# Kernel optimization log

Measured on AMD Instinct MI355X. Metric: run time of the kernel, lower is better.

Reference implementation:

```python
import jax, jax.numpy as jnp
import numpy as np

EPS = 1e-5  # BatchNorm eps; eval mode with default running stats (mean=0, var=1)


def _bn(h, gamma, beta):
    # eval-mode BatchNorm2d with running_mean=0, running_var=1
    scale = gamma / jnp.sqrt(1.0 + EPS)
    return h * scale[None, :, None, None] + beta[None, :, None, None]


def _conv1x1(h, w, b):
    # 1x1 conv == channel matmul. h: [B,C,H,W], w: [O,C], b: [O]
    return jnp.einsum('bchw,oc->bohw', h, w) + b[None, :, None, None]


def setup_inputs() -> dict:
    key = jax.random.key(0)
    ks = jax.random.split(key, 16)
    B, C, H, W = 8, 64, 64, 64
    inp = {
        'x': jax.random.normal(ks[0], (B, C, H, W), dtype=jnp.float32),
        'saliency_map': jax.random.uniform(ks[1], (B, H, W), dtype=jnp.float32),
    }
    i = 2
    for name in ('q', 'k', 'v'):
        inp[f'w_{name}'] = jax.random.normal(ks[i], (C, C), dtype=jnp.float32) * (1.0 / np.sqrt(C)); i += 1
        inp[f'b_{name}'] = jax.random.normal(ks[i], (C,), dtype=jnp.float32) * 0.02; i += 1
        inp[f'g_{name}'] = 1.0 + 0.1 * jax.random.normal(ks[i], (C,), dtype=jnp.float32); i += 1
        inp[f'be_{name}'] = jax.random.normal(ks[i], (C,), dtype=jnp.float32) * 0.02; i += 1
    inp['g_o'] = 1.0 + 0.1 * jax.random.normal(ks[14], (C,), dtype=jnp.float32)
    inp['be_o'] = jax.random.normal(ks[15], (C,), dtype=jnp.float32) * 0.02
    return inp


def reference(x, saliency_map, w_q, b_q, g_q, be_q, w_k, b_k, g_k, be_k,
              w_v, b_v, g_v, be_v, g_o, be_o):
    B, C, H, W = x.shape
    HW = H * W
    query = _bn(_conv1x1(x, w_q, b_q), g_q, be_q).reshape(B, C, HW)
    key_ = _bn(_conv1x1(x, w_k, b_k), g_k, be_k).reshape(B, C, HW)
    value = _bn(_conv1x1(x, w_v, b_v), g_v, be_v).reshape(B, C, HW)
    mask = saliency_map.reshape(B, 1, HW)  # broadcast over channels == repeat
    query = query * mask
    # scores[b,i,j] = sum_c q[b,c,i] * k[b,c,j]; softmax over j (no scaling)
    scores = jnp.einsum('bci,bcj->bij', query, key_)
    attn = jax.nn.softmax(scores, axis=-1)
    # out[b,c,j] = sum_i v[b,c,i] * attn[b,i,j]
    enhanced = jnp.einsum('bci,bij->bcj', value, attn).reshape(B, C, H, W)
    enhanced = enhanced + x
    return _bn(enhanced, g_o, be_o)
```

## Files before the change

### kernel.cpp

```cpp
#include <hip/hip_runtime.h>

#define EPS 1e-5f
#define LOG2E 1.4426950408889634f

typedef __attribute__((ext_vector_type(8)))  short    s8b;
typedef __attribute__((ext_vector_type(4)))  short    s4b;
typedef __attribute__((ext_vector_type(16))) float    f32x16;
typedef __attribute__((ext_vector_type(4)))  float    f32x4;
typedef __attribute__((ext_vector_type(4)))  unsigned u32x4;

__device__ __forceinline__ unsigned cvt_pk_bf16(float lo, float hi) {
    unsigned r;
    asm("v_cvt_pk_bf16_f32 %0, %1, %2" : "=v"(r) : "v"(lo), "v"(hi));
    return r;
}
__device__ __forceinline__ void permswap(unsigned &a, unsigned &b) {
    asm("v_permlane32_swap_b32 %0, %1" : "+v"(a), "+v"(b));
}
union PackAB { u32x4 u; s8b s; };

__device__ __forceinline__ unsigned short f2bf(float f) {
    union { float f; unsigned u; } v; v.f = f;
    unsigned r = v.u + 0x7FFFu + ((v.u >> 16) & 1u);
    return (unsigned short)(r >> 16);
}
__device__ __forceinline__ float bf2f(unsigned short h) {
    union { unsigned u; float f; } v; v.u = ((unsigned)h) << 16;
    return v.f;
}


__global__ __launch_bounds__(256) void qkv_kernel(
    const float* __restrict__ x, const float* __restrict__ sal,
    const float* __restrict__ wq, const float* __restrict__ bq,
    const float* __restrict__ gq, const float* __restrict__ beq,
    const float* __restrict__ wk, const float* __restrict__ bk,
    const float* __restrict__ gk, const float* __restrict__ bek,
    const float* __restrict__ wv, const float* __restrict__ bv,
    const float* __restrict__ gv, const float* __restrict__ bev,
    short* __restrict__ Qf, short* __restrict__ Kf, short* __restrict__ Vf)
{
    __shared__ short wbf[6][4096];
    __shared__ short xbf[4096];
    __shared__ short v_lds[4096];
    __shared__ float sc_lds[3][64];
    __shared__ float bb_lds[3][64];

    const int t = threadIdx.x;
    const int b = blockIdx.x & 7;
    const int p0 = (blockIdx.x >> 3) * 64;

    if (t < 192) {
        int m = t >> 6, o = t & 63;
        const float* g  = (m == 0) ? gq  : (m == 1) ? gk  : gv;
        const float* be = (m == 0) ? beq : (m == 1) ? bek : bev;
        const float* bi = (m == 0) ? bq  : (m == 1) ? bk  : bv;
        float lam = (m == 0) ? LOG2E : 1.0f;
        float s = g[o] * rsqrtf(1.0f + EPS) * lam;
        sc_lds[m][o] = s;
        bb_lds[m][o] = bi[o] * s + be[o] * lam;
    }
    __syncthreads();

    for (int rep = 0; rep < 12; ++rep) {
        int idx = (rep * 256 + t) * 4;
        int m = idx >> 12;
        int r = idx & 4095;
        int o = r >> 6, c0 = r & 63;
        const float* w = (m == 0) ? wq : (m == 1) ? wk : wv;
        float4 v4 = *reinterpret_cast<const float4*>(w + r);
        float s = sc_lds[m][o];
        float w0 = v4.x * s, w1 = v4.y * s, w2 = v4.z * s, w3 = v4.w * s;
        unsigned short h0 = f2bf(w0), h1 = f2bf(w1), h2 = f2bf(w2), h3 = f2bf(w3);
        s4b hv, lv;
        hv[0] = (short)h0; hv[1] = (short)h1; hv[2] = (short)h2; hv[3] = (short)h3;
        lv[0] = (short)f2bf(w0 - bf2f(h0));
        lv[1] = (short)f2bf(w1 - bf2f(h1));
        lv[2] = (short)f2bf(w2 - bf2f(h2));
        lv[3] = (short)f2bf(w3 - bf2f(h3));
        int sidx = (o * 64 + c0) ^ ((o & 7) << 3);
        *reinterpret_cast<s4b*>(&wbf[m * 2 + 0][sidx]) = hv;
        *reinterpret_cast<s4b*>(&wbf[m * 2 + 1][sidx]) = lv;
    }
    {
        const int xp = t & 63;
        const int cgrp = (t >> 6) * 4;
        const float* xb = x + ((size_t)(b * 64) << 12) + p0 + xp;
        for (int rep = 0; rep < 4; ++rep) {
            int cb = cgrp + rep * 16;
            float x0 = xb[(size_t)(cb + 0) << 12];
            float x1 = xb[(size_t)(cb + 1) << 12];
            float x2 = xb[(size_t)(cb + 2) << 12];
            float x3 = xb[(size_t)(cb + 3) << 12];
            s4b pk;
            pk[0] = (short)f2bf(x0); pk[1] = (short)f2bf(x1);
            pk[2] = (short)f2bf(x2); pk[3] = (short)f2bf(x3);
            int sidx = (xp * 64 + cb) ^ ((xp & 7) << 3);
            *reinterpret_cast<s4b*>(&xbf[sidx]) = pk;
        }
    }
    __syncthreads();

    const int lane = t & 63, wave = t >> 6;
    const int l31 = lane & 31, hi = lane >> 5;
    const int phalf = wave & 1, ohalf = wave >> 1;
    const int prow = phalf * 32 + l31;
    const int orow = ohalf * 32 + l31;
    const int ib = (p0 >> 5) + phalf;
    const int swz = (l31 & 7) << 3;

    s8b bx[4];
#pragma unroll
    for (int s = 0; s < 4; ++s)
        bx[s] = *reinterpret_cast<const s8b*>(
            &xbf[(prow * 64 + s * 16 + hi * 8) ^ ((prow & 7) << 3)]);

    const float msk = sal[(((size_t)b) << 12) + p0 + prow];

#pragma unroll
    for (int m = 0; m < 3; ++m) {
        s8b ah[4], al[4];
#pragma unroll
        for (int s = 0; s < 4; ++s) {
            int sidx = (orow * 64 + s * 16 + hi * 8) ^ swz;
            ah[s] = *reinterpret_cast<const s8b*>(&wbf[m * 2 + 0][sidx]);
            al[s] = *reinterpret_cast<const s8b*>(&wbf[m * 2 + 1][sidx]);
        }
        f32x16 d;
#pragma unroll
        for (int r = 0; r < 16; ++r) d[r] = 0.f;
#pragma unroll
        for (int s = 0; s < 4; ++s)
            d = __builtin_amdgcn_mfma_f32_32x32x16_bf16(ah[s], bx[s], d, 0, 0, 0);
#pragma unroll
        for (int s = 0; s < 4; ++s)
            d = __builtin_amdgcn_mfma_f32_32x32x16_bf16(al[s], bx[s], d, 0, 0, 0);

        float pv[16];
#pragma unroll
        for (int g = 0; g < 4; ++g) {
            f32x4 bb = *reinterpret_cast<const f32x4*>(
                &bb_lds[m][ohalf * 32 + 8 * g + 4 * hi]);
#pragma unroll
            for (int q = 0; q < 4; ++q) pv[g * 4 + q] = d[g * 4 + q] + bb[q];
        }
        if (m == 0) {
#pragma unroll
            for (int r = 0; r < 16; ++r) pv[r] *= msk;
        }
        if (m < 2) {
            unsigned a0 = cvt_pk_bf16(pv[0],  pv[1]);
            unsigned a1 = cvt_pk_bf16(pv[2],  pv[3]);
            unsigned a2 = cvt_pk_bf16(pv[4],  pv[5]);
            unsigned a3 = cvt_pk_bf16(pv[6],  pv[7]);
            unsigned b0 = cvt_pk_bf16(pv[8],  pv[9]);
            unsigned b1 = cvt_pk_bf16(pv[10], pv[11]);
            unsigned b2 = cvt_pk_bf16(pv[12], pv[13]);
            unsigned b3 = cvt_pk_bf16(pv[14], pv[15]);
            permswap(a0, a2); permswap(a1, a3);
            permswap(b0, b2); permswap(b1, b3);
            PackAB pa0, pa1;
            pa0.u.x = a0; pa0.u.y = a1; pa0.u.z = a2; pa0.u.w = a3;
            pa1.u.x = b0; pa1.u.y = b1; pa1.u.z = b2; pa1.u.w = b3;
            short* dst = (m == 0) ? Qf : Kf;
            size_t base =
                ((((size_t)(b * 128 + ib) * 4 + ohalf * 2) * 2 + hi) * 32 + l31) * 8;
            *reinterpret_cast<u32x4*>(dst + base)       = pa0.u;
            *reinterpret_cast<u32x4*>(dst + base + 512) = pa1.u;
        } else {
#pragma unroll
            for (int r = 0; r < 16; ++r) {
                int c = ohalf * 32 + (r & 3) + 8 * (r >> 2) + 4 * hi;
                int sidx = (c * 64 + prow) ^ ((c & 7) << 3);
                v_lds[sidx] = (short)f2bf(pv[r]);
            }
        }
    }
    __syncthreads();

    const size_t vbase = (size_t)(b * 128 + (p0 >> 5)) * 2048;
#pragma unroll
    for (int r = 0; r < 2; ++r) {
        int f = r * 256 + t;
        int c = f & 63;
        int iL = ((f >> 6) & 7) * 8;
        int sidx = (c * 64 + iL) ^ ((c & 7) << 3);
        u32x4 val = *reinterpret_cast<const u32x4*>(&v_lds[sidx]);
        *reinterpret_cast<u32x4*>(Vf + vbase + (size_t)f * 8) = val;
    }
}

#define LOADK(JB, DST) {                                                      \
    const short* _kp = Kf +                                                   \
        ((((size_t)(b * 128 + (JB)) * 4) * 2 + hi) * 32 + l31) * 8;           \
    DST[0] = *reinterpret_cast<const s8b*>(_kp);                              \
    DST[1] = *reinterpret_cast<const s8b*>(_kp + 512);                        \
    DST[2] = *reinterpret_cast<const s8b*>(_kp + 1024);                       \
    DST[3] = *reinterpret_cast<const s8b*>(_kp + 1536); }

#define RBODY(KARR) {                                                         \
    f32x16 sacc;                                                              \
    _Pragma("unroll") for (int r = 0; r < 16; ++r) sacc[r] = 0.f;             \
    __builtin_amdgcn_s_setprio(1);                                            \
    _Pragma("unroll") for (int s = 0; s < 4; ++s)                             \
        sacc = __builtin_amdgcn_mfma_f32_32x32x16_bf16(qf[s], KARR[s], sacc, 0, 0, 0); \
    __builtin_amdgcn_s_setprio(0);                                            \
    _Pragma("unroll") for (int r = 0; r < 16; ++r)                            \
        lsum[r] += __builtin_exp2f(sacc[r]); }

__global__ __launch_bounds__(512, 2) void rowsum_kernel(
    const short* __restrict__ Qf, const short* __restrict__ Kf,
    float* __restrict__ inv_l)
{
    __shared__ float part[8][32];

    const int t = threadIdx.x;
    const int b = blockIdx.x & 7;
    const int it2 = blockIdx.x >> 3;
    const int wave = t >> 6, lane = t & 63;
    const int wi = wave & 1, wj = wave >> 1;
    const int l31 = lane & 31, hi = lane >> 5;

    const short* qp = Qf +
        ((((size_t)(b * 128 + it2 * 2 + wi) * 4) * 2 + hi) * 32 + l31) * 8;
    s8b qf[4];
#pragma unroll
    for (int s = 0; s < 4; ++s)
        qf[s] = *reinterpret_cast<const s8b*>(qp + s * 512);

    float lsum[16];
#pragma unroll
    for (int r = 0; r < 16; ++r) lsum[r] = 0.f;

    s8b kA[4], kB[4];
    LOADK(wj, kA);
    for (int jj = 0; jj < 32; jj += 2) {
        LOADK((jj + 1) * 4 + wj, kB);
        RBODY(kA);
        if (jj + 2 < 32) { LOADK((jj + 2) * 4 + wj, kA); }
        RBODY(kB);
    }

#pragma unroll
    for (int off = 1; off < 32; off <<= 1)
#pragma unroll
        for (int r = 0; r < 16; ++r) lsum[r] += __shfl_xor(lsum[r], off);

    if (l31 == 0) {
#pragma unroll
        for (int r = 0; r < 16; ++r) {
            int iloc = (r & 3) + 8 * (r >> 2) + 4 * hi;
            part[wave][iloc] = lsum[r];
        }
    }
    __syncthreads();
    if (t < 64) {
        int wi_t = t >> 5, row = t & 31;
        float s = part[wi_t][row] + part[2 + wi_t][row] +
                  part[4 + wi_t][row] + part[6 + wi_t][row];
        inv_l[(((size_t)b) << 12) + it2 * 64 + wi_t * 32 + row] = 1.0f / s;
    }
}

#define LOADQ(IB, DST) {                                                      \
    const short* _qp = Qf +                                                   \
        ((((size_t)(b * 128 + (IB)) * 4) * 2 + hi) * 32 + l31) * 8;           \
    DST[0] = *reinterpret_cast<const s8b*>(_qp);                              \
    DST[1] = *reinterpret_cast<const s8b*>(_qp + 512);                        \
    DST[2] = *reinterpret_cast<const s8b*>(_qp + 1024);                       \
    DST[3] = *reinterpret_cast<const s8b*>(_qp + 1536); }

#define LOADV(IB, DST) {                                                      \
    const short* _vp = Vf +                                                   \
        ((((size_t)(b * 128 + (IB)) * 2) * 2 + hi) * 64 + l31) * 8;           \
    DST[0] = *reinterpret_cast<const s8b*>(_vp);                              \
    DST[1] = *reinterpret_cast<const s8b*>(_vp + 256);                        \
    DST[2] = *reinterpret_cast<const s8b*>(_vp + 1024);                       \
    DST[3] = *reinterpret_cast<const s8b*>(_vp + 1280); }

#define ABODY(QARR, VARR, IB) {                                               \
    f32x16 sacc;                                                              \
    _Pragma("unroll") for (int r = 0; r < 16; ++r) sacc[r] = 0.f;             \
    __builtin_amdgcn_s_setprio(1);                                            \
    _Pragma("unroll") for (int s = 0; s < 4; ++s)                             \
        sacc = __builtin_amdgcn_mfma_f32_32x32x16_bf16(QARR[s], kf[s], sacc, 0, 0, 0); \
    __builtin_amdgcn_s_setprio(0);                                            \
    float p[16];                                                              \
    const int _ibase = (IB) * 32 + 4 * hi;                                    \
    _Pragma("unroll") for (int g = 0; g < 4; ++g) {                           \
        f32x4 li = *reinterpret_cast<const f32x4*>(lip + _ibase + 8 * g);     \
        _Pragma("unroll") for (int q = 0; q < 4; ++q)                         \
            p[g * 4 + q] = __builtin_exp2f(sacc[g * 4 + q]) * li[q];          \
    }                                                                         \
    unsigned a0 = cvt_pk_bf16(p[0],  p[1]),  a1 = cvt_pk_bf16(p[2],  p[3]);   \
    unsigned a2 = cvt_pk_bf16(p[4],  p[5]),  a3 = cvt_pk_bf16(p[6],  p[7]);   \
    unsigned b0 = cvt_pk_bf16(p[8],  p[9]),  b1 = cvt_pk_bf16(p[10], p[11]);  \
    unsigned b2 = cvt_pk_bf16(p[12], p[13]), b3 = cvt_pk_bf16(p[14], p[15]);  \
    permswap(a0, a2); permswap(a1, a3); permswap(b0, b2); permswap(b1, b3);   \
    PackAB pa0, pa1;                                                          \
    pa0.u.x = a0; pa0.u.y = a1; pa0.u.z = a2; pa0.u.w = a3;                   \
    pa1.u.x = b0; pa1.u.y = b1; pa1.u.z = b2; pa1.u.w = b3;                   \
    __builtin_amdgcn_s_setprio(1);                                            \
    acc0 = __builtin_amdgcn_mfma_f32_32x32x16_bf16(pa0.s, VARR[0], acc0, 0, 0, 0); \
    acc1 = __builtin_amdgcn_mfma_f32_32x32x16_bf16(pa0.s, VARR[1], acc1, 0, 0, 0); \
    acc0 = __builtin_amdgcn_mfma_f32_32x32x16_bf16(pa1.s, VARR[2], acc0, 0, 0, 0); \
    acc1 = __builtin_amdgcn_mfma_f32_32x32x16_bf16(pa1.s, VARR[3], acc1, 0, 0, 0); \
    __builtin_amdgcn_s_setprio(0); }

__global__ __launch_bounds__(512, 2) void attnout_kernel(
    const short* __restrict__ Qf, const short* __restrict__ Kf,
    const short* __restrict__ Vf, const float* __restrict__ inv_l,
    const float* __restrict__ x, const float* __restrict__ go,
    const float* __restrict__ beo, float* __restrict__ out)
{
    __shared__ float red[2][3][64][33];

    const int t = threadIdx.x;
    const int b = blockIdx.x & 7;
    const int jt = blockIdx.x >> 3;
    const int wave = t >> 6, lane = t & 63;
    const int wr = wave >> 1;
    const int wc = wave & 1;
    const int l31 = lane & 31, hi = lane >> 5;

    const short* kp = Kf +
        ((((size_t)(b * 128 + jt * 2 + wc) * 4) * 2 + hi) * 32 + l31) * 8;
    s8b kf[4];
#pragma unroll
    for (int s = 0; s < 4; ++s)
        kf[s] = *reinterpret_cast<const s8b*>(kp + s * 512);

    f32x16 acc0, acc1;
#pragma unroll
    for (int r = 0; r < 16; ++r) { acc0[r] = 0.f; acc1[r] = 0.f; }

    const float* lip = inv_l + (((size_t)b) << 12);

    s8b qA[4], qB[4], vA[4], vB[4];
    LOADQ(wr, qA);
    LOADV(wr, vA);
    for (int ii = 0; ii < 32; ii += 2) {
        const int ibA = ii * 4 + wr;
        const int ibB = ibA + 4;
        LOADQ(ibB, qB);
        LOADV(ibB, vB);
        ABODY(qA, vA, ibA);
        if (ii + 2 < 32) { LOADQ(ibA + 8, qA); LOADV(ibA + 8, vA); }
        ABODY(qB, vB, ibB);
    }

    if (wr > 0) {
#pragma unroll
        for (int nf = 0; nf < 2; ++nf) {
            const f32x16& A = nf ? acc1 : acc0;
            int c = nf * 32 + l31;
#pragma unroll
            for (int g = 0; g < 4; ++g) {
                f32x4 v;
                v.x = A[g * 4 + 0]; v.y = A[g * 4 + 1];
                v.z = A[g * 4 + 2]; v.w = A[g * 4 + 3];
                *reinterpret_cast<f32x4*>(&red[wc][wr - 1][c][g * 8 + 4 * hi]) = v;
            }
        }
    }
    __syncthreads();
    if (wr == 0) {
#pragma unroll
        for (int nf = 0; nf < 2; ++nf) {
            const f32x16& A = nf ? acc1 : acc0;
            int c = nf * 32 + l31;
            const float sc = go[c] * rsqrtf(1.0f + EPS);
            const float bb = beo[c];
            size_t rowb = (((size_t)(b * 64 + c)) << 12) + jt * 64 + wc * 32;
#pragma unroll
            for (int g = 0; g < 4; ++g) {
                int jl = g * 8 + 4 * hi;
                f32x4 p0 = *reinterpret_cast<const f32x4*>(&red[wc][0][c][jl]);
                f32x4 p1 = *reinterpret_cast<const f32x4*>(&red[wc][1][c][jl]);
                f32x4 p2 = *reinterpret_cast<const f32x4*>(&red[wc][2][c][jl]);
                f32x4 xv = *reinterpret_cast<const f32x4*>(x + rowb + jl);
                f32x4 ov;
                ov.x = (A[g * 4 + 0] + p0.x + p1.x + p2.x + xv.x) * sc + bb;
                ov.y = (A[g * 4 + 1] + p0.y + p1.y + p2.y + xv.y) * sc + bb;
                ov.z = (A[g * 4 + 2] + p0.z + p1.z + p2.z + xv.z) * sc + bb;
                ov.w = (A[g * 4 + 3] + p0.w + p1.w + p2.w + xv.w) * sc + bb;
                *reinterpret_cast<f32x4*>(out + rowb + jl) = ov;
            }
        }
    }
}

extern "C" void kernel_launch(void* const* d_in, const int* in_sizes, int n_in,
                              void* d_out, int out_size, void* d_ws, size_t ws_size,
                              hipStream_t stream)
{
    (void)in_sizes; (void)n_in; (void)out_size; (void)ws_size;
    const float* x   = (const float*)d_in[0];
    const float* sal = (const float*)d_in[1];
    const float* wq  = (const float*)d_in[2];  const float* bq  = (const float*)d_in[3];
    const float* gq  = (const float*)d_in[4];  const float* beq = (const float*)d_in[5];
    const float* wk  = (const float*)d_in[6];  const float* bk  = (const float*)d_in[7];
    const float* gk  = (const float*)d_in[8];  const float* bek = (const float*)d_in[9];
    const float* wv  = (const float*)d_in[10]; const float* bv  = (const float*)d_in[11];
    const float* gv  = (const float*)d_in[12]; const float* bev = (const float*)d_in[13];
    const float* go  = (const float*)d_in[14]; const float* beo = (const float*)d_in[15];
    float* out = (float*)d_out;

    short* ws = (short*)d_ws;
    short* Qf = ws;
    short* Kf = ws + 2097152;
    short* Vf = ws + 4194304;
    float* il = (float*)(ws + 6291456);

    qkv_kernel<<<512, 256, 0, stream>>>(x, sal, wq, bq, gq, beq,
                                        wk, bk, gk, bek, wv, bv, gv, bev,
                                        Qf, Kf, Vf);
    rowsum_kernel<<<512, 512, 0, stream>>>(Qf, Kf, il);
    attnout_kernel<<<512, 512, 0, stream>>>(Qf, Kf, Vf, il, x, go, beo, out);
}
```

Measured before the change: 199.9 us.

## Simplify attention loops, drop setprio and manual prefetch, reshape rowsum blocks

The rowsum kernel now uses 256-thread blocks with one query tile per block and four waves splitting the key range, launched as 1024 blocks. The attnout kernel drops its hand-written double-buffered Q/V register prefetch and s_setprio hints in favour of a plain per-iteration load loop, and raises the launch bounds to 4 blocks per CU. The intent is to lower register pressure and raise occupancy so the hardware hides latency instead of software prefetch. The risk is exposed global-load latency inside the loop, and spills if the compiler cannot fit the tighter register budget.

After: 196.4 us. No clear change (-1.7%).

```diff
diff --git a/kernel.cpp b/kernel.cpp
--- a/kernel.cpp
+++ b/kernel.cpp
@@ -201,28 +201,26 @@
 #define RBODY(KARR) {                                                         \
     f32x16 sacc;                                                              \
     _Pragma("unroll") for (int r = 0; r < 16; ++r) sacc[r] = 0.f;             \
-    __builtin_amdgcn_s_setprio(1);                                            \
     _Pragma("unroll") for (int s = 0; s < 4; ++s)                             \
         sacc = __builtin_amdgcn_mfma_f32_32x32x16_bf16(qf[s], KARR[s], sacc, 0, 0, 0); \
-    __builtin_amdgcn_s_setprio(0);                                            \
     _Pragma("unroll") for (int r = 0; r < 16; ++r)                            \
         lsum[r] += __builtin_exp2f(sacc[r]); }
 
-__global__ __launch_bounds__(512, 2) void rowsum_kernel(
+__global__ __launch_bounds__(256, 4) void rowsum_kernel(
     const short* __restrict__ Qf, const short* __restrict__ Kf,
     float* __restrict__ inv_l)
 {
-    __shared__ float part[8][32];
+    __shared__ float part[4][32];
 
     const int t = threadIdx.x;
     const int b = blockIdx.x & 7;
-    const int it2 = blockIdx.x >> 3;
+    const int it = blockIdx.x >> 3;
     const int wave = t >> 6, lane = t & 63;
-    const int wi = wave & 1, wj = wave >> 1;
+    const int wj = wave;
     const int l31 = lane & 31, hi = lane >> 5;
 
     const short* qp = Qf +
-        ((((size_t)(b * 128 + it2 * 2 + wi) * 4) * 2 + hi) * 32 + l31) * 8;
+        ((((size_t)(b * 128 + it) * 4) * 2 + hi) * 32 + l31) * 8;
     s8b qf[4];
 #pragma unroll
     for (int s = 0; s < 4; ++s)
@@ -254,60 +252,12 @@
         }
     }
     __syncthreads();
-    if (t < 64) {
-        int wi_t = t >> 5, row = t & 31;
-        float s = part[wi_t][row] + part[2 + wi_t][row] +
-                  part[4 + wi_t][row] + part[6 + wi_t][row];
-        inv_l[(((size_t)b) << 12) + it2 * 64 + wi_t * 32 + row] = 1.0f / s;
-    }
-}
-
-#define LOADQ(IB, DST) {                                                      \
-    const short* _qp = Qf +                                                   \
-        ((((size_t)(b * 128 + (IB)) * 4) * 2 + hi) * 32 + l31) * 8;           \
-    DST[0] = *reinterpret_cast<const s8b*>(_qp);                              \
-    DST[1] = *reinterpret_cast<const s8b*>(_qp + 512);                        \
-    DST[2] = *reinterpret_cast<const s8b*>(_qp + 1024);                       \
-    DST[3] = *reinterpret_cast<const s8b*>(_qp + 1536); }
-
-#define LOADV(IB, DST) {                                                      \
-    const short* _vp = Vf +                                                   \
-        ((((size_t)(b * 128 + (IB)) * 2) * 2 + hi) * 64 + l31) * 8;           \
-    DST[0] = *reinterpret_cast<const s8b*>(_vp);                              \
-    DST[1] = *reinterpret_cast<const s8b*>(_vp + 256);                        \
-    DST[2] = *reinterpret_cast<const s8b*>(_vp + 1024);                       \
-    DST[3] = *reinterpret_cast<const s8b*>(_vp + 1280); }
-
-#define ABODY(QARR, VARR, IB) {                                               \
-    f32x16 sacc;                                                              \
-    _Pragma("unroll") for (int r = 0; r < 16; ++r) sacc[r] = 0.f;             \
-    __builtin_amdgcn_s_setprio(1);                                            \
-    _Pragma("unroll") for (int s = 0; s < 4; ++s)                             \
-        sacc = __builtin_amdgcn_mfma_f32_32x32x16_bf16(QARR[s], kf[s], sacc, 0, 0, 0); \
-    __builtin_amdgcn_s_setprio(0);                                            \
-    float p[16];                                                              \
-    const int _ibase = (IB) * 32 + 4 * hi;                                    \
-    _Pragma("unroll") for (int g = 0; g < 4; ++g) {                           \
-        f32x4 li = *reinterpret_cast<const f32x4*>(lip + _ibase + 8 * g);     \
-        _Pragma("unroll") for (int q = 0; q < 4; ++q)                         \
-            p[g * 4 + q] = __builtin_exp2f(sacc[g * 4 + q]) * li[q];          \
-    }                                                                         \
-    unsigned a0 = cvt_pk_bf16(p[0],  p[1]),  a1 = cvt_pk_bf16(p[2],  p[3]);   \
-    unsigned a2 = cvt_pk_bf16(p[4],  p[5]),  a3 = cvt_pk_bf16(p[6],  p[7]);   \
-    unsigned b0 = cvt_pk_bf16(p[8],  p[9]),  b1 = cvt_pk_bf16(p[10], p[11]);  \
-    unsigned b2 = cvt_pk_bf16(p[12], p[13]), b3 = cvt_pk_bf16(p[14], p[15]);  \
-    permswap(a0, a2); permswap(a1, a3); permswap(b0, b2); permswap(b1, b3);   \
-    PackAB pa0, pa1;                                                          \
-    pa0.u.x = a0; pa0.u.y = a1; pa0.u.z = a2; pa0.u.w = a3;                   \
-    pa1.u.x = b0; pa1.u.y = b1; pa1.u.z = b2; pa1.u.w = b3;                   \
-    __builtin_amdgcn_s_setprio(1);                                            \
-    acc0 = __builtin_amdgcn_mfma_f32_32x32x16_bf16(pa0.s, VARR[0], acc0, 0, 0, 0); \
-    acc1 = __builtin_amdgcn_mfma_f32_32x32x16_bf16(pa0.s, VARR[1], acc1, 0, 0, 0); \
-    acc0 = __builtin_amdgcn_mfma_f32_32x32x16_bf16(pa1.s, VARR[2], acc0, 0, 0, 0); \
-    acc1 = __builtin_amdgcn_mfma_f32_32x32x16_bf16(pa1.s, VARR[3], acc1, 0, 0, 0); \
-    __builtin_amdgcn_s_setprio(0); }
-
-__global__ __launch_bounds__(512, 2) void attnout_kernel(
+    if (t < 32)
+        inv_l[(((size_t)b) << 12) + it * 32 + t] =
+            1.0f / (part[0][t] + part[1][t] + part[2][t] + part[3][t]);
+}
+
+__global__ __launch_bounds__(512, 4) void attnout_kernel(
     const short* __restrict__ Qf, const short* __restrict__ Kf,
     const short* __restrict__ Vf, const float* __restrict__ inv_l,
     const float* __restrict__ x, const float* __restrict__ go,
@@ -336,17 +286,62 @@
 
     const float* lip = inv_l + (((size_t)b) << 12);
 
-    s8b qA[4], qB[4], vA[4], vB[4];
-    LOADQ(wr, qA);
-    LOADV(wr, vA);
-    for (int ii = 0; ii < 32; ii += 2) {
-        const int ibA = ii * 4 + wr;
-        const int ibB = ibA + 4;
-        LOADQ(ibB, qB);
-        LOADV(ibB, vB);
-        ABODY(qA, vA, ibA);
-        if (ii + 2 < 32) { LOADQ(ibA + 8, qA); LOADV(ibA + 8, vA); }
-        ABODY(qB, vB, ibB);
+    for (int ii = 0; ii < 32; ++ii) {
+        const int ib = ii * 4 + wr;
+        const short* qp = Qf +
+            ((((size_t)(b * 128 + ib) * 4) * 2 + hi) * 32 + l31) * 8;
+        s8b qf[4];
+#pragma unroll
+        for (int s = 0; s < 4; ++s)
+            qf[s] = *reinterpret_cast<const s8b*>(qp + s * 512);
+
+        const short* vp = Vf +
+            ((((size_t)(b * 128 + ib) * 2) * 2 + hi) * 64 + l31) * 8;
+        s8b vf[2][2];
+#pragma unroll
+        for (int s2 = 0; s2 < 2; ++s2)
+#pragma unroll
+            for (int nf = 0; nf < 2; ++nf)
+                vf[s2][nf] = *reinterpret_cast<const s8b*>(
+                    vp + s2 * 1024 + nf * 256);
+
+        f32x4 li[4];
+#pragma unroll
+        for (int g = 0; g < 4; ++g)
+            li[g] = *reinterpret_cast<const f32x4*>(lip + ib * 32 + 4 * hi + 8 * g);
+
+        f32x16 sacc;
+#pragma unroll
+        for (int r = 0; r < 16; ++r) sacc[r] = 0.f;
+#pragma unroll
+        for (int s = 0; s < 4; ++s)
+            sacc = __builtin_amdgcn_mfma_f32_32x32x16_bf16(qf[s], kf[s], sacc, 0, 0, 0);
+
+        float p[16];
+#pragma unroll
+        for (int g = 0; g < 4; ++g)
+#pragma unroll
+            for (int q = 0; q < 4; ++q)
+                p[g * 4 + q] = __builtin_exp2f(sacc[g * 4 + q]) * li[g][q];
+
+        unsigned a0 = cvt_pk_bf16(p[0],  p[1]);
+        unsigned a1 = cvt_pk_bf16(p[2],  p[3]);
+        unsigned a2 = cvt_pk_bf16(p[4],  p[5]);
+        unsigned a3 = cvt_pk_bf16(p[6],  p[7]);
+        unsigned b0 = cvt_pk_bf16(p[8],  p[9]);
+        unsigned b1 = cvt_pk_bf16(p[10], p[11]);
+        unsigned b2 = cvt_pk_bf16(p[12], p[13]);
+        unsigned b3 = cvt_pk_bf16(p[14], p[15]);
+        permswap(a0, a2); permswap(a1, a3);
+        permswap(b0, b2); permswap(b1, b3);
+        PackAB pa0, pa1;
+        pa0.u.x = a0; pa0.u.y = a1; pa0.u.z = a2; pa0.u.w = a3;
+        pa1.u.x = b0; pa1.u.y = b1; pa1.u.z = b2; pa1.u.w = b3;
+
+        acc0 = __builtin_amdgcn_mfma_f32_32x32x16_bf16(pa0.s, vf[0][0], acc0, 0, 0, 0);
+        acc1 = __builtin_amdgcn_mfma_f32_32x32x16_bf16(pa0.s, vf[0][1], acc1, 0, 0, 0);
+        acc0 = __builtin_amdgcn_mfma_f32_32x32x16_bf16(pa1.s, vf[1][0], acc0, 0, 0, 0);
+        acc1 = __builtin_amdgcn_mfma_f32_32x32x16_bf16(pa1.s, vf[1][1], acc1, 0, 0, 0);
     }
 
     if (wr > 0) {
@@ -415,6 +410,6 @@
     qkv_kernel<<<512, 256, 0, stream>>>(x, sal, wq, bq, gq, beq,
                                         wk, bk, gk, bek, wv, bv, gv, bev,
                                         Qf, Kf, Vf);
-    rowsum_kernel<<<512, 512, 0, stream>>>(Qf, Kf, il);
+    rowsum_kernel<<<1024, 256, 0, stream>>>(Qf, Kf, il);
     attnout_kernel<<<512, 512, 0, stream>>>(Qf, Kf, Vf, il, x, go, beo, out);
 }
```
